# Kernel tuning notes

Hardware: AMD Instinct MI355X
Metric: run time of the kernel (lower is better)

## Reference

```python
import jax, jax.numpy as jnp
import numpy as np

NF, D, H, HD, NL, FF = 5, 64, 8, 8, 2, 128   # features, d_model, heads, head_dim, layers, ffn
NQ, QL, NC = 8, 3, 3                          # qubits, quantum layers, classes


def pos_encoding(S, d):
    pos = np.arange(S, dtype=np.float32)[:, None]
    div = np.exp(np.arange(0, d, 2, dtype=np.float32) * (-np.log(10000.0) / d))
    pe = np.zeros((S, d), np.float32)
    pe[:, 0::2] = np.sin(pos * div)
    pe[:, 1::2] = np.cos(pos * div)
    return jnp.asarray(pe)


def layernorm(x, g, b, eps=1e-5):
    m = x.mean(-1, keepdims=True)
    v = ((x - m) ** 2).mean(-1, keepdims=True)
    return (x - m) * jax.lax.rsqrt(v + eps) * g + b


def apply1q(psi, U, w):
    # psi: (2,)*NQ complex state; apply 2x2 gate U on wire w
    p = jnp.moveaxis(psi, w, 0)
    sh = p.shape
    p = (U @ p.reshape(2, -1)).reshape(sh)
    return jnp.moveaxis(p, 0, w)


def cnot(psi, c, t):
    p = jnp.moveaxis(psi, (c, t), (0, 1))
    sh = p.shape
    p = p.reshape(2, 2, -1)
    p = jnp.stack([p[0], p[1, ::-1]], 0).reshape(sh)  # flip target when control=1
    return jnp.moveaxis(p, (0, 1), (c, t))


def rx_mat(t):
    c, s = jnp.cos(t / 2), jnp.sin(t / 2)
    return jnp.stack([jnp.stack([c + 0j, -1j * s]), jnp.stack([-1j * s, c + 0j])]).astype(jnp.complex64)


def rot_mat(phi, th, om):
    # qml.Rot = RZ(om) RY(th) RZ(phi)
    c, s = jnp.cos(th / 2), jnp.sin(th / 2)
    return jnp.stack([
        jnp.stack([jnp.exp(-0.5j * (phi + om)) * c, -jnp.exp(0.5j * (phi - om)) * s]),
        jnp.stack([jnp.exp(-0.5j * (phi - om)) * s, jnp.exp(0.5j * (phi + om)) * c]),
    ]).astype(jnp.complex64)


def quantum_circuit(angles, weights):
    # angles: [NQ], weights: [QL, NQ, 3]. Circuit: QL x (AngleEmbedding(RX) + StronglyEntanglingLayer(range=1))
    psi = jnp.zeros((2,) * NQ, jnp.complex64).at[(0,) * NQ].set(1.0)
    for l in range(QL):
        for w in range(NQ):
            psi = apply1q(psi, rx_mat(angles[w]), w)
        for w in range(NQ):
            psi = apply1q(psi, rot_mat(weights[l, w, 0], weights[l, w, 1], weights[l, w, 2]), w)
        for w in range(NQ):
            psi = cnot(psi, w, (w + 1) % NQ)
    prob = jnp.abs(psi) ** 2
    zs = []
    for w in range(NC):  # <Z_w> = p(0_w) - p(1_w)
        marg = prob.sum(axis=tuple(i for i in range(NQ) if i != w))
        zs.append(marg[0] - marg[1])
    # von Neumann entropy of wires 0..3 (trace out wires 4..7), natural log
    mat = psi.reshape(16, 16)
    rho = mat @ mat.conj().T
    ev = jnp.clip(jnp.linalg.eigvalsh(rho), 1e-10, 1.0)
    ent = -jnp.sum(ev * jnp.log(ev))
    return jnp.stack(zs), ent


def setup_inputs() -> dict:
    key = jax.random.key(0)
    ks = jax.random.split(key, 30)
    sc = 0.02
    inp = {
        'x': jax.random.normal(ks[0], (16, 1024, NF), jnp.float32),
        'Wemb': sc * jax.random.normal(ks[1], (NF, D)), 'bemb': jnp.zeros((D,)),
        'Wq': sc * jax.random.normal(ks[2], (NL, D, D)), 'bq': jnp.zeros((NL, D)),
        'Wk': sc * jax.random.normal(ks[3], (NL, D, D)), 'bk': jnp.zeros((NL, D)),
        'Wv': sc * jax.random.normal(ks[4], (NL, D, D)), 'bv': jnp.zeros((NL, D)),
        'Wo': sc * jax.random.normal(ks[5], (NL, D, D)), 'bo': jnp.zeros((NL, D)),
        'ln1g': jnp.ones((NL, D)), 'ln1b': jnp.zeros((NL, D)),
        'ln2g': jnp.ones((NL, D)), 'ln2b': jnp.zeros((NL, D)),
        'Wf1': sc * jax.random.normal(ks[6], (NL, D, FF)), 'bf1': jnp.zeros((NL, FF)),
        'Wf2': sc * jax.random.normal(ks[7], (NL, FF, D)), 'bf2': jnp.zeros((NL, D)),
        'Wp1': sc * jax.random.normal(ks[8], (D, 32)), 'bp1': jnp.zeros((32,)),
        'Wp2': sc * jax.random.normal(ks[9], (32, NQ)), 'bp2': jnp.zeros((NQ,)),
        'qweights': jax.random.normal(ks[10], (QL, NQ, 3)),
    }
    return inp


def reference(x, Wemb, bemb, Wq, bq, Wk, bk, Wv, bv, Wo, bo, ln1g, ln1b, ln2g, ln2b,
              Wf1, bf1, Wf2, bf2, Wp1, bp1, Wp2, bp2, qweights):
    B, S, _ = x.shape
    h = x @ Wemb + bemb + pos_encoding(S, D)[None]  # aug + dropout are identity in eval
    scale = np.float32(1.0 / np.sqrt(HD))
    for l in range(NL):
        q = (h @ Wq[l] + bq[l]).reshape(B, S, H, HD).transpose(0, 2, 1, 3)
        k = (h @ Wk[l] + bk[l]).reshape(B, S, H, HD).transpose(0, 2, 1, 3)
        v = (h @ Wv[l] + bv[l]).reshape(B, S, H, HD).transpose(0, 2, 1, 3)
        att = jax.nn.softmax(jnp.einsum('bhsd,bhtd->bhst', q, k) * scale, axis=-1)
        o = jnp.einsum('bhst,bhtd->bhsd', att, v).transpose(0, 2, 1, 3).reshape(B, S, D)
        h = layernorm(h + o @ Wo[l] + bo[l], ln1g[l], ln1b[l])
        ff = jax.nn.relu(h @ Wf1[l] + bf1[l]) @ Wf2[l] + bf2[l]
        h = layernorm(h + ff, ln2g[l], ln2b[l])
    pooled = h.mean(1)
    feats = jax.nn.relu(pooled @ Wp1 + bp1) @ Wp2 + bp2
    angles = jnp.tanh(feats) * np.float32(np.pi)
    logits, ent = jax.vmap(quantum_circuit, in_axes=(0, None))(angles, qweights)
    return logits, ent
```

## Files before the change

### kernel.cpp

```cpp
#include <hip/hip_runtime.h>
#include <math.h>

#define BB 16
#define SS 1024
#define NF 5
#define DD 64
#define HH 8
#define HDIM 8
#define NLAYER 2
#define FFD 128
#define NQ 8
#define QLAY 3
#define NC 3
#define NSWEEP 5

typedef __fp16 hf2 __attribute__((ext_vector_type(2)));
typedef __fp16 h8  __attribute__((ext_vector_type(8)));
typedef float  f4x __attribute__((ext_vector_type(4)));

__device__ __forceinline__ int   f2i_(float x) { union { float f; int i; } u; u.f = x; return u.i; }
__device__ __forceinline__ float i2f_(int x)   { union { float f; int i; } u; u.i = x; return u.f; }

__device__ __forceinline__ float bperm_(int pa, float x) {
    return i2f_(__builtin_amdgcn_ds_bpermute(pa, f2i_(x)));
}

__device__ __forceinline__ float half32_(float x) {
#if defined(__has_builtin)
#if __has_builtin(__builtin_amdgcn_permlane32_swap)
    int xi = f2i_(x);
    auto r = __builtin_amdgcn_permlane32_swap(xi, xi, false, false);
    int r0 = (int)r[0], r1 = (int)r[1];
    return i2f_(r0 == xi ? r1 : r0);
#else
    return __shfl_xor(x, 32);
#endif
#else
    return __shfl_xor(x, 32);
#endif
}

template<int M> __device__ __forceinline__ float lx(float x) {
    if constexpr (M == 0) {
        return x;
    } else if constexpr (M == 1) {
        return i2f_(__builtin_amdgcn_update_dpp(0, f2i_(x), 0xB1, 0xF, 0xF, true));
    } else if constexpr (M == 2) {
        return i2f_(__builtin_amdgcn_update_dpp(0, f2i_(x), 0x4E, 0xF, 0xF, true));
    } else if constexpr (M == 3) {
        return i2f_(__builtin_amdgcn_update_dpp(0, f2i_(x), 0x1B, 0xF, 0xF, true));
    } else if constexpr (M < 32) {
        return i2f_(__builtin_amdgcn_ds_swizzle(f2i_(x), (M << 10) | 0x1F));
    } else {
        return lx<M & 31>(half32_(x));
    }
}

__device__ __forceinline__ float half16_(float x) {
#if defined(__has_builtin)
#if __has_builtin(__builtin_amdgcn_permlane16_swap)
    int xi = f2i_(x);
    auto r = __builtin_amdgcn_permlane16_swap(xi, xi, false, false);
    int r0 = (int)r[0], r1 = (int)r[1];
    return i2f_(r0 == xi ? r1 : r0);
#else
    return lx<16>(x);
#endif
#else
    return lx<16>(x);
#endif
}

__device__ __forceinline__ float wsum64_(float v) {
    v += half32_(v);
    v += half16_(v);
    v += lx<8>(v);
    v += lx<4>(v);
    v += lx<2>(v);
    v += lx<1>(v);
    return v;
}

#if defined(__has_builtin)
#if __has_builtin(__builtin_amdgcn_exp2f)
#define EXP2F(x) __builtin_amdgcn_exp2f(x)
#else
#define EXP2F(x) exp2f(x)
#endif
#else
#define EXP2F(x) exp2f(x)
#endif

#define QSCALE (0.3535533906f * 1.4426950408889634f)

__global__ __launch_bounds__(64) void k_qkv0(const float* __restrict__ x,
                                             const float* __restrict__ Wemb,
                                             const float* __restrict__ bemb,
                                             const float* __restrict__ Wq, const float* __restrict__ bq,
                                             const float* __restrict__ Wk, const float* __restrict__ bk,
                                             const float* __restrict__ Wv, const float* __restrict__ bv,
                                             hf2* __restrict__ qh, hf2* __restrict__ kh,
                                             hf2* __restrict__ vt, float* __restrict__ h) {
    __shared__ float hrow[4][DD];
    int d   = threadIdx.x;
    int bs0 = blockIdx.x * 4;
    {
        int i = d >> 1;
        float div = expf((float)(2 * i) * (-9.210340371976184f / 64.0f));
#pragma unroll
        for (int r = 0; r < 4; ++r) {
            int bs = bs0 + r;
            int s  = bs & (SS - 1);
            const float* xr = x + bs * NF;
            float acc = bemb[d];
#pragma unroll
            for (int f = 0; f < NF; ++f) acc += xr[f] * Wemb[f * DD + d];
            float ang = (float)s * div;
            float pe = (d & 1) ? cosf(ang) : sinf(ang);
            float hv = acc + pe;
            hrow[r][d] = hv;
            h[bs * DD + d] = hv;
        }
    }
    __syncthreads();
    const float* wq = Wq;
    const float* wk = Wk;
    const float* wv = Wv;
    float aq[4], ak[4], av[4];
    float bqv = bq[d], bkv = bk[d], bvv = bv[d];
#pragma unroll
    for (int r = 0; r < 4; ++r) { aq[r] = bqv; ak[r] = bkv; av[r] = bvv; }
#pragma unroll 4
    for (int i = 0; i < DD; ++i) {
        float wqv = wq[i * DD + d], wkv = wk[i * DD + d], wvv = wv[i * DD + d];
#pragma unroll
        for (int r = 0; r < 4; ++r) {
            float hv = hrow[r][i];
            aq[r] += hv * wqv; ak[r] += hv * wkv; av[r] += hv * wvv;
        }
    }
    int hh = d >> 3, hd = d & 7;
    const float qs = QSCALE;
    float aqp[4], akp[4];
#pragma unroll
    for (int r = 0; r < 4; ++r) { aqp[r] = lx<1>(aq[r]); akp[r] = lx<1>(ak[r]); }
    if ((hd & 1) == 0) {
#pragma unroll
        for (int r = 0; r < 4; ++r) {
            int bs = bs0 + r;
            int b = bs >> 10, s = bs & 1023;
            int bhs = ((b * HH + hh) << 10) | s;
            qh[bhs * 4 + (hd >> 1)] = __builtin_amdgcn_cvt_pkrtz(aq[r] * qs, aqp[r] * qs);
            kh[bhs * 4 + (hd >> 1)] = __builtin_amdgcn_cvt_pkrtz(ak[r], akp[r]);
        }
    }
    {
        int b = bs0 >> 10, s0 = bs0 & 1023;
        int vrow = (b * HH + hh) * 8 + hd;
        hf2* vp = vt + vrow * 512 + (s0 >> 1);
        vp[0] = __builtin_amdgcn_cvt_pkrtz(av[0], av[1]);
        vp[1] = __builtin_amdgcn_cvt_pkrtz(av[2], av[3]);
    }
}

__global__ __launch_bounds__(256) void k_attn(const float4* __restrict__ qh4,
                                              const float4* __restrict__ kh4,
                                              const float4* __restrict__ vt4,
                                              float* __restrict__ Ao) {
    int bh  = blockIdx.x;
    int sb  = blockIdx.y;
    int tid = threadIdx.x;
    int wv  = tid >> 6;
    int L   = tid & 63;
    int m = L & 15, quad = L >> 4;
    union U { float4 f; h8 h; };
    h8 hz = {0,0,0,0,0,0,0,0};
    h8 bQ = hz;
    if (quad == 0) { U u; u.f = qh4[(bh << 10) | (sb * 64 + wv * 16 + m)]; bQ = u.h; }
    int kmap = 8 * (m >> 2) + (m & 3);
    const float4* kbase = kh4 + (bh << 10);
    const float4* vbase = vt4 + ((bh * 8 + (m & 7)) << 7);
    f4x Oacc = {0.f, 0.f, 0.f, 0.f};
    float ls = 0.f;
    for (int kc = 0; kc < 32; ++kc) {
        h8 aK0 = hz, aK1 = hz;
        if (quad == 0) {
            U u0, u1;
            u0.f = kbase[kc * 32 + kmap];
            u1.f = kbase[kc * 32 + kmap + 4];
            aK0 = u0.h; aK1 = u1.h;
        }
        f4x S0 = {0.f,0.f,0.f,0.f}, S1 = {0.f,0.f,0.f,0.f};
        S0 = __builtin_amdgcn_mfma_f32_16x16x32_f16(aK0, bQ, S0, 0, 0, 0);
        S1 = __builtin_amdgcn_mfma_f32_16x16x32_f16(aK1, bQ, S1, 0, 0, 0);
        float p0 = EXP2F(S0[0]), p1 = EXP2F(S0[1]);
        float p2 = EXP2F(S0[2]), p3 = EXP2F(S0[3]);
        float p4 = EXP2F(S1[0]), p5 = EXP2F(S1[1]);
        float p6 = EXP2F(S1[2]), p7 = EXP2F(S1[3]);
        ls += (p0 + p1 + p2 + p3) + (p4 + p5 + p6 + p7);
        hf2 c0 = __builtin_amdgcn_cvt_pkrtz(p0, p1);
        hf2 c1 = __builtin_amdgcn_cvt_pkrtz(p2, p3);
        hf2 c2 = __builtin_amdgcn_cvt_pkrtz(p4, p5);
        hf2 c3 = __builtin_amdgcn_cvt_pkrtz(p6, p7);
        h8 aP;
        aP[0] = c0[0]; aP[1] = c0[1]; aP[2] = c1[0]; aP[3] = c1[1];
        aP[4] = c2[0]; aP[5] = c2[1]; aP[6] = c3[0]; aP[7] = c3[1];
        h8 bV = hz;
        if (m < 8) {
            U uv; uv.f = vbase[kc * 4 + quad];
            bV = uv.h;
        }
        Oacc = __builtin_amdgcn_mfma_f32_16x16x32_f16(aP, bV, Oacc, 0, 0, 0);
    }
    ls += half16_(ls);
    ls += half32_(ls);
    float d0 = bperm_((4 * quad + 0) << 2, ls);
    float d1 = bperm_((4 * quad + 1) << 2, ls);
    float d2 = bperm_((4 * quad + 2) << 2, ls);
    float d3 = bperm_((4 * quad + 3) << 2, ls);
    if (m < 8) {
        int srow = sb * 64 + wv * 16 + quad * 4;
        int base = (((bh << 10) | srow) << 3) + m;
        Ao[base]      = Oacc[0] / d0;
        Ao[base + 8]  = Oacc[1] / d1;
        Ao[base + 16] = Oacc[2] / d2;
        Ao[base + 24] = Oacc[3] / d3;
    }
}

__global__ __launch_bounds__(128) void k_mid(const float* __restrict__ Ao,
                                             const float* __restrict__ Wo, const float* __restrict__ bo,
                                             const float* __restrict__ g1, const float* __restrict__ b1,
                                             const float* __restrict__ Wf1, const float* __restrict__ bf1,
                                             const float* __restrict__ Wf2, const float* __restrict__ bf2,
                                             const float* __restrict__ g2, const float* __restrict__ b2,
                                             float* __restrict__ h, int l, int fuse,
                                             const float* __restrict__ Wq, const float* __restrict__ bq,
                                             const float* __restrict__ Wk, const float* __restrict__ bk,
                                             const float* __restrict__ Wv, const float* __restrict__ bv,
                                             hf2* __restrict__ qh, hf2* __restrict__ kh,
                                             hf2* __restrict__ vt, float* __restrict__ pp2) {
    __shared__ float orow[4][DD];
    __shared__ float h1s[4][DD];
    __shared__ float frow[4][FFD];
    __shared__ float hfin[4][DD];
    int t    = threadIdx.x;
    int d    = t & 63;
    int half = t >> 6;
    int bs0  = blockIdx.x * 4;
    int hh = d >> 3, hd = d & 7;
    int r0 = half * 2, r1 = r0 + 1;

#pragma unroll
    for (int rr = 0; rr < 2; ++rr) {
        int r  = r0 + rr;
        int bs = bs0 + r;
        int b = bs >> 10, s = bs & 1023;
        int bhs = ((b * HH + hh) << 10) | s;
        orow[r][d] = Ao[(bhs << 3) + hd];
    }
    __syncthreads();

    {
        const float* w = Wo + l * DD * DD;
        float bias = bo[l * DD + d];
        float acc0 = bias, acc1 = bias;
#pragma unroll 4
        for (int i = 0; i < DD; ++i) {
            float wv = w[i * DD + d];
            acc0 += orow[r0][i] * wv;
            acc1 += orow[r1][i] * wv;
        }
        float gg = g1[l * DD + d], bb = b1[l * DD + d];
        float accs[2] = {acc0, acc1};
#pragma unroll
        for (int rr = 0; rr < 2; ++rr) {
            int r = r0 + rr;
            float a = accs[rr] + h[(bs0 + r) * DD + d];
            float sum = wsum64_(a);
            float mean = sum * (1.f / 64.f);
            float dx = a - mean;
            float vs = wsum64_(dx * dx);
            float rstd = rsqrtf(vs * (1.f / 64.f) + 1e-5f);
            h1s[r][d] = dx * rstd * gg + bb;
        }
    }
    __syncthreads();

    {
        const float* w = Wf1 + l * DD * FFD;
        float bv_ = bf1[l * FFD + t];
        float a0 = bv_, a1 = bv_, a2 = bv_, a3 = bv_;
#pragma unroll 4
        for (int i = 0; i < DD; ++i) {
            float wv = w[i * FFD + t];
            a0 += h1s[0][i]*wv; a1 += h1s[1][i]*wv;
            a2 += h1s[2][i]*wv; a3 += h1s[3][i]*wv;
        }
        frow[0][t] = fmaxf(a0, 0.f); frow[1][t] = fmaxf(a1, 0.f);
        frow[2][t] = fmaxf(a2, 0.f); frow[3][t] = fmaxf(a3, 0.f);
    }
    __syncthreads();

    {
        const float* w = Wf2 + l * FFD * DD;
        float bias = bf2[l * DD + d];
        float acc0 = bias, acc1 = bias;
#pragma unroll 4
        for (int i = 0; i < FFD; ++i) {
            float wv = w[i * DD + d];
            acc0 += frow[r0][i] * wv;
            acc1 += frow[r1][i] * wv;
        }
        float gg = g2[l * DD + d], bb = b2[l * DD + d];
        float accs[2] = {acc0, acc1};
#pragma unroll
        for (int rr = 0; rr < 2; ++rr) {
            int r = r0 + rr;
            float a = accs[rr] + h1s[r][d];
            float sum = wsum64_(a);
            float mean = sum * (1.f / 64.f);
            float dx = a - mean;
            float vs = wsum64_(dx * dx);
            float rstd = rsqrtf(vs * (1.f / 64.f) + 1e-5f);
            float hv = dx * rstd * gg + bb;
            hfin[r][d] = hv;
            h[(bs0 + r) * DD + d] = hv;
        }
    }

    if (!fuse) {
        __syncthreads();
        if (t < 64) {
            pp2[blockIdx.x * DD + t] = (hfin[0][t] + hfin[1][t]) + (hfin[2][t] + hfin[3][t]);
        }
        return;
    }

    __syncthreads();
    const int l1 = l + 1;
    if (t < 64) {
        const float* wq = Wq + l1 * DD * DD;
        const float* wk = Wk + l1 * DD * DD;
        float aq[4], ak[4];
        float bqv = bq[l1 * DD + d], bkv = bk[l1 * DD + d];
#pragma unroll
        for (int r = 0; r < 4; ++r) { aq[r] = bqv; ak[r] = bkv; }
#pragma unroll 4
        for (int i = 0; i < DD; ++i) {
            float wqv = wq[i * DD + d], wkv = wk[i * DD + d];
#pragma unroll
            for (int r = 0; r < 4; ++r) {
                float hv = hfin[r][i];
                aq[r] += hv * wqv; ak[r] += hv * wkv;
            }
        }
        const float qs = QSCALE;
        float aqp[4], akp[4];
#pragma unroll
        for (int r = 0; r < 4; ++r) { aqp[r] = lx<1>(aq[r]); akp[r] = lx<1>(ak[r]); }
        if ((hd & 1) == 0) {
#pragma unroll
            for (int r = 0; r < 4; ++r) {
                int bs = bs0 + r;
                int b = bs >> 10, s = bs & 1023;
                int bhs = ((b * HH + hh) << 10) | s;
                qh[bhs * 4 + (hd >> 1)] = __builtin_amdgcn_cvt_pkrtz(aq[r] * qs, aqp[r] * qs);
                kh[bhs * 4 + (hd >> 1)] = __builtin_amdgcn_cvt_pkrtz(ak[r], akp[r]);
            }
        }
    } else {
        const float* wv = Wv + l1 * DD * DD;
        float av[4];
        float bvv = bv[l1 * DD + d];
#pragma unroll
        for (int r = 0; r < 4; ++r) av[r] = bvv;
#pragma unroll 4
        for (int i = 0; i < DD; ++i) {
            float wvv = wv[i * DD + d];
#pragma unroll
            for (int r = 0; r < 4; ++r) av[r] += hfin[r][i] * wvv;
        }
        int b = bs0 >> 10, s0 = bs0 & 1023;
        int vrow = (b * HH + hh) * 8 + hd;
        hf2* vp = vt + vrow * 512 + (s0 >> 1);
        vp[0] = __builtin_amdgcn_cvt_pkrtz(av[0], av[1]);
        vp[1] = __builtin_amdgcn_cvt_pkrtz(av[2], av[3]);
    }
}

__global__ __launch_bounds__(256) void k_tail(const float* __restrict__ pp2,
                                              const float* __restrict__ Wp1, const float* __restrict__ bp1,
                                              const float* __restrict__ Wp2, const float* __restrict__ bp2,
                                              const float* __restrict__ qw,
                                              float* __restrict__ out) {
    __shared__ float part[4][DD];
    __shared__ float pool_s[DD];
    __shared__ float hid[32];
    __shared__ float ang_s[NQ];
    __shared__ float ucoef[QLAY * 16][8];
    __shared__ float2 Ps2[256];
    int b = blockIdx.x; int t = threadIdx.x;
    int L = t;
    int lb4 = (t & 63) << 2;

    {
        int d = t & 63, ch = t >> 6;
        const float* pp = pp2 + (b * 256 + ch * 64) * DD + d;
        float acc = 0.f;
#pragma unroll 8
        for (int j = 0; j < 64; ++j) acc += pp[j * DD];
        part[ch][d] = acc;
    }
    __syncthreads();
    if (t < 64) pool_s[t] = (part[0][t] + part[1][t] + part[2][t] + part[3][t]) * (1.f / 1024.f);
    __syncthreads();
    if (t < 32) {
        float a = bp1[t];
#pragma unroll 8
        for (int i = 0; i < DD; ++i) a += pool_s[i] * Wp1[i * 32 + t];
        hid[t] = fmaxf(a, 0.f);
    }
    __syncthreads();
    if (t < NQ) {
        float a = bp2[t];
#pragma unroll 8
        for (int j = 0; j < 32; ++j) a += hid[j] * Wp2[j * NQ + t];
        ang_s[t] = tanhf(a) * 3.14159265358979f;
    }
    __syncthreads();

    if (t < QLAY * 16) {
        int l = t >> 4, g8 = t & 15, w = g8 & 7;
        float u00r, u00i, u01r, u01i, u10r, u10i, u11r, u11i;
        if (g8 < 8) {
            float ha = 0.5f * ang_s[w];
            float c = __cosf(ha), s = __sinf(ha);
            u00r = c;   u00i = 0.f; u01r = 0.f; u01i = -s;
            u10r = 0.f; u10i = -s;  u11r = c;   u11i = 0.f;
        } else {
            const float* p3 = qw + (l * NQ + w) * 3;
            float phi = p3[0], th = p3[1], om = p3[2];
            float ct = __cosf(0.5f * th), st = __sinf(0.5f * th);
            float al = 0.5f * (phi + om), be = 0.5f * (phi - om);
            float ca = __cosf(al), sa = __sinf(al), cb = __cosf(be), sb = __sinf(be);
            u00r =  ct * ca; u00i = -ct * sa;
            u01r = -st * cb; u01i = -st * sb;
            u10r =  st * cb; u10i = -st * sb;
            u11r =  ct * ca; u11i =  ct * sa;
        }
        float* up = ucoef[t];
        up[0] = u00r; up[1] = u00i; up[2] = u01r; up[3] = u01i;
        up[4] = u10r; up[5] = u10i; up[6] = u11r; up[7] = u11i;
    }
    __syncthreads();

    float ar[4], ai[4];
#pragma unroll
    for (int r = 0; r < 4; ++r) { ar[r] = 0.f; ai[r] = 0.f; }
    if (L == 0) ar[0] = 1.f;

    if (t < 64) {
#pragma unroll 1
        for (int l = 0; l < QLAY; ++l) {
#pragma unroll 1
            for (int g8 = 0; g8 < 16; ++g8) {
                const float* up = ucoef[(l << 4) | g8];
                float u00r = up[0], u00i = up[1], u01r = up[2], u01i = up[3];
                float u10r = up[4], u10i = up[5], u11r = up[6], u11i = up[7];
                int p = 7 - (g8 & 7);
                if (p >= 6) {
#pragma unroll
                    for (int pi_ = 0; pi_ < 2; ++pi_) {
                        int lo = (p == 7) ? pi_ : pi_ * 2;
                        int hi = (p == 7) ? pi_ + 2 : pi_ * 2 + 1;
                        float r0 = ar[lo], m0 = ai[lo], r1 = ar[hi], m1 = ai[hi];
                        ar[lo] = u00r*r0 - u00i*m0 + u01r*r1 - u01i*m1;
                        ai[lo] = u00r*m0 + u00i*r0 + u01r*m1 + u01i*r1;
                        ar[hi] = u10r*r0 - u10i*m0 + u11r*r1 - u11i*m1;
                        ai[hi] = u10r*m0 + u10i*r0 + u11r*m1 + u11i*r1;
                    }
                } else {
                    int bit = (L >> p) & 1;
                    float car = bit ? u11r : u00r, cai = bit ? u11i : u00i;
                    float cpr = bit ? u10r : u01r, cpi = bit ? u10i : u01i;
                    float pre[4], pim[4];
                    if (p == 5) {
#pragma unroll
                        for (int r = 0; r < 4; ++r) { pre[r] = half32_(ar[r]); pim[r] = half32_(ai[r]); }
                    } else if (p == 4) {
#pragma unroll
                        for (int r = 0; r < 4; ++r) { pre[r] = half16_(ar[r]); pim[r] = half16_(ai[r]); }
                    } else if (p == 3) {
#pragma unroll
                        for (int r = 0; r < 4; ++r) { pre[r] = lx<8>(ar[r]); pim[r] = lx<8>(ai[r]); }
                    } else if (p == 2) {
#pragma unroll
                        for (int r = 0; r < 4; ++r) { pre[r] = lx<4>(ar[r]); pim[r] = lx<4>(ai[r]); }
                    } else if (p == 1) {
#pragma unroll
                        for (int r = 0; r < 4; ++r) { pre[r] = lx<2>(ar[r]); pim[r] = lx<2>(ai[r]); }
                    } else {
#pragma unroll
                        for (int r = 0; r < 4; ++r) { pre[r] = lx<1>(ar[r]); pim[r] = lx<1>(ai[r]); }
                    }
#pragma unroll
                    for (int r = 0; r < 4; ++r) {
                        float nr = car*ar[r] - cai*ai[r] + cpr*pre[r] - cpi*pim[r];
                        float ni = car*ai[r] + cai*ar[r] + cpr*pim[r] + cpi*pre[r];
                        ar[r] = nr; ai[r] = ni;
                    }
                }
            }
            { float t0=ar[2]; ar[2]=ar[3]; ar[3]=t0; t0=ai[2]; ai[2]=ai[3]; ai[3]=t0; }
            ar[1] = half32_(ar[1]); ai[1] = half32_(ai[1]);
            ar[3] = half32_(ar[3]); ai[3] = half32_(ai[3]);
#pragma unroll 1
            for (int w = 2; w <= 6; ++w) {
                int pc = 7 - w, pt = 6 - w;
                bool ctrl = (L >> pc) & 1;
                float swr[4], swi[4];
                if (pt == 4) {
#pragma unroll
                    for (int r = 0; r < 4; ++r) { swr[r] = half16_(ar[r]); swi[r] = half16_(ai[r]); }
                } else if (pt == 3) {
#pragma unroll
                    for (int r = 0; r < 4; ++r) { swr[r] = lx<8>(ar[r]); swi[r] = lx<8>(ai[r]); }
                } else if (pt == 2) {
#pragma unroll
                    for (int r = 0; r < 4; ++r) { swr[r] = lx<4>(ar[r]); swi[r] = lx<4>(ai[r]); }
                } else if (pt == 1) {
#pragma unroll
                    for (int r = 0; r < 4; ++r) { swr[r] = lx<2>(ar[r]); swi[r] = lx<2>(ai[r]); }
                } else {
#pragma unroll
                    for (int r = 0; r < 4; ++r) { swr[r] = lx<1>(ar[r]); swi[r] = lx<1>(ai[r]); }
                }
#pragma unroll
                for (int r = 0; r < 4; ++r) {
                    ar[r] = ctrl ? swr[r] : ar[r];
                    ai[r] = ctrl ? swi[r] : ai[r];
                }
            }
            {
                bool ctrl = L & 1;
                float n0r = ctrl ? ar[2] : ar[0], n2r = ctrl ? ar[0] : ar[2];
                float n0i = ctrl ? ai[2] : ai[0], n2i = ctrl ? ai[0] : ai[2];
                float n1r = ctrl ? ar[3] : ar[1], n3r = ctrl ? ar[1] : ar[3];
                float n1i = ctrl ? ai[3] : ai[1], n3i = ctrl ? ai[1] : ai[3];
                ar[0]=n0r; ar[1]=n1r; ar[2]=n2r; ar[3]=n3r;
                ai[0]=n0i; ai[1]=n1i; ai[2]=n2i; ai[3]=n3i;
            }
        }

        {
            float p0 = ar[0]*ar[0]+ai[0]*ai[0];
            float p1 = ar[1]*ar[1]+ai[1]*ai[1];
            float p2 = ar[2]*ar[2]+ai[2]*ai[2];
            float p3 = ar[3]*ar[3]+ai[3]*ai[3];
            float z0 = p0 + p1 - p2 - p3;
            float z1 = p0 - p1 + p2 - p3;
            float zs = p0 + p1 + p2 + p3;
            float z2 = (L & 32) ? -zs : zs;
            z0 += lx<1>(z0);   z1 += lx<1>(z1);   z2 += lx<1>(z2);
            z0 += lx<2>(z0);   z1 += lx<2>(z1);   z2 += lx<2>(z2);
            z0 += lx<4>(z0);   z1 += lx<4>(z1);   z2 += lx<4>(z2);
            z0 += lx<8>(z0);   z1 += lx<8>(z1);   z2 += lx<8>(z2);
            z0 += half16_(z0); z1 += half16_(z1); z2 += half16_(z2);
            z0 += half32_(z0); z1 += half32_(z1); z2 += half32_(z2);
            if (L == 0) {
                out[b * NC + 0] = z0;
                out[b * NC + 1] = z1;
                out[b * NC + 2] = z2;
            }
        }

#pragma unroll
        for (int r = 0; r < 4; ++r) Ps2[(r << 6) | L] = make_float2(ar[r], ai[r]);
    }
    __syncthreads();

    if (t < 64) {
        int c   = L >> 2;
        int seg = L & 3;
        float gr[4], gi[4];
#pragma unroll
        for (int j = 0; j < 4; ++j) {
            float2 tv = Ps2[(seg * 4 + j) * 16 + c];
            gr[j] = tv.x; gi[j] = tv.y;
        }
        float alm = 0.f;
#pragma unroll
        for (int j = 0; j < 4; ++j) alm += gr[j]*gr[j] + gi[j]*gi[j];
        alm += lx<1>(alm);
        alm += lx<2>(alm);

#pragma unroll 1
        for (int sweep = 0; sweep < NSWEEP; ++sweep) {
#pragma unroll 1
            for (int m = 1; m <= 15; ++m) {
                int xm = m << 2;
                float pgr[4], pgi[4], bep;
                if ((xm & 12) == 0) {
                    if (xm == 16) {
#pragma unroll
                        for (int j = 0; j < 4; ++j) { pgr[j] = half16_(gr[j]); pgi[j] = half16_(gi[j]); }
                        bep = half16_(alm);
                    } else if (xm == 32) {
#pragma unroll
                        for (int j = 0; j < 4; ++j) { pgr[j] = half32_(gr[j]); pgi[j] = half32_(gi[j]); }
                        bep = half32_(alm);
                    } else {
#pragma unroll
                        for (int j = 0; j < 4; ++j) {
                            pgr[j] = half16_(half32_(gr[j]));
                            pgi[j] = half16_(half32_(gi[j]));
                        }
                        bep = half16_(half32_(alm));
                    }
                } else {
                    int pa = lb4 ^ (xm << 2);
#pragma unroll
                    for (int j = 0; j < 4; ++j) {
                        pgr[j] = bperm_(pa, gr[j]);
                        pgi[j] = bperm_(pa, gi[j]);
                    }
                    bep = bperm_(pa, alm);
                }
                float d = 0.f, e = 0.f;
#pragma unroll
                for (int j = 0; j < 4; ++j) {
                    d += gr[j]*pgr[j] + gi[j]*pgi[j];
                    e += gr[j]*pgi[j] - gi[j]*pgr[j];
                }
                d += lx<1>(d); e += lx<1>(e);
                d += lx<2>(d); e += lx<2>(e);
                float g2 = d*d + e*e;
                float cth = 1.f, sth = 0.f, cph = 1.f, sph = 0.f, gn = 0.f;
                if (g2 > 1e-26f) {
                    gn = __builtin_amdgcn_sqrtf(g2);
                    float ginv = __builtin_amdgcn_rcpf(gn);
                    cph = d * ginv; sph = -e * ginv;
                    float tau = (alm - bep) * (0.5f * ginv);
                    float rr = __builtin_amdgcn_rsqf(1.f + tau*tau);
                    float co = fminf(fabsf(tau) * rr, 1.0f);
                    cth = __builtin_amdgcn_sqrtf(0.5f + 0.5f*co);
                    sth = copysignf(__builtin_amdgcn_sqrtf(0.5f - 0.5f*co), tau);
                }
#pragma unroll
                for (int j = 0; j < 4; ++j) {
                    float er = cph*pgr[j] - sph*pgi[j];
                    float ei = cph*pgi[j] + sph*pgr[j];
                    gr[j] = cth * gr[j] + sth * er;
                    gi[j] = cth * gi[j] + sth * ei;
                }
                alm = cth*cth*alm + sth*sth*bep + 2.f*cth*sth*gn;
            }
        }

        float alm2 = 0.f;
#pragma unroll
        for (int j = 0; j < 4; ++j) alm2 += gr[j]*gr[j] + gi[j]*gi[j];
        alm2 += lx<1>(alm2);
        alm2 += lx<2>(alm2);

        float ev = fminf(fmaxf(alm2, 1e-10f), 1.0f);
        float term = -ev * __logf(ev);
        term += lx<4>(term);
        term += lx<8>(term);
        term += half16_(term);
        term += half32_(term);
        if (L == 0) out[BB * NC + b] = term;
    }
}

extern "C" void kernel_launch(void* const* d_in, const int* in_sizes, int n_in,
                              void* d_out, int out_size, void* d_ws, size_t ws_size,
                              hipStream_t stream) {
    const float* x    = (const float*)d_in[0];
    const float* Wemb = (const float*)d_in[1];
    const float* bemb = (const float*)d_in[2];
    const float* Wq   = (const float*)d_in[3];
    const float* bq   = (const float*)d_in[4];
    const float* Wk   = (const float*)d_in[5];
    const float* bk   = (const float*)d_in[6];
    const float* Wv   = (const float*)d_in[7];
    const float* bv   = (const float*)d_in[8];
    const float* Wo   = (const float*)d_in[9];
    const float* bo   = (const float*)d_in[10];
    const float* ln1g = (const float*)d_in[11];
    const float* ln1b = (const float*)d_in[12];
    const float* ln2g = (const float*)d_in[13];
    const float* ln2b = (const float*)d_in[14];
    const float* Wf1  = (const float*)d_in[15];
    const float* bf1  = (const float*)d_in[16];
    const float* Wf2  = (const float*)d_in[17];
    const float* bf2  = (const float*)d_in[18];
    const float* Wp1  = (const float*)d_in[19];
    const float* bp1  = (const float*)d_in[20];
    const float* Wp2  = (const float*)d_in[21];
    const float* bp2  = (const float*)d_in[22];
    const float* qwts = (const float*)d_in[23];
    float* out = (float*)d_out;

    const size_t M = 1u << 20;
    float* ws   = (float*)d_ws;
    float* h    = ws;
    hf2*   qh   = (hf2*)(ws + M);
    hf2*   kh   = (hf2*)(ws + M + M / 2);
    hf2*   vt   = (hf2*)(ws + 2 * M);
    float* Ao   = ws + 2 * M + M / 2;
    float* pp2  = ws + 3 * M + M / 2;

    k_qkv0<<<BB * SS / 4, 64, 0, stream>>>(x, Wemb, bemb, Wq, bq, Wk, bk, Wv, bv,
                                           qh, kh, vt, h);
    k_attn<<<dim3(BB * HH, 16), 256, 0, stream>>>((const float4*)qh, (const float4*)kh,
                                                  (const float4*)vt, Ao);
    k_mid<<<BB * SS / 4, 128, 0, stream>>>(Ao, Wo, bo, ln1g, ln1b,
                                           Wf1, bf1, Wf2, bf2, ln2g, ln2b, h, 0, 1,
                                           Wq, bq, Wk, bk, Wv, bv, qh, kh, vt, pp2);
    k_attn<<<dim3(BB * HH, 16), 256, 0, stream>>>((const float4*)qh, (const float4*)kh,
                                                  (const float4*)vt, Ao);
    k_mid<<<BB * SS / 4, 128, 0, stream>>>(Ao, Wo, bo, ln1g, ln1b,
                                           Wf1, bf1, Wf2, bf2, ln2g, ln2b, h, 1, 0,
                                           Wq, bq, Wk, bk, Wv, bv, qh, kh, vt, pp2);
    k_tail<<<BB, 256, 0, stream>>>(pp2, Wp1, bp1, Wp2, bp2, qwts, out);
}
```

Baseline: 292.4 us.

## Run tail kernel as single 1024-thread block with one wavefront per batch

The tail kernel changes from 16 blocks of 256 threads to one block of 1024 threads, with each 64-lane wavefront handling one batch element. The pooling reduction now uses float4 loads and cross-lane reductions instead of a shared-memory partial-sum stage, and no lanes sit idle during the quantum simulation. This reduces per-block overhead and idle threads, but puts all the tail work on a single compute unit, which may add latency where 16 blocks previously ran in parallel across CUs.

```diff
diff --git a/kernel.cpp b/kernel.cpp
--- a/kernel.cpp
+++ b/kernel.cpp
@@ -389,52 +389,61 @@
     }
 }
 
-__global__ __launch_bounds__(256) void k_tail(const float* __restrict__ pp2,
-                                              const float* __restrict__ Wp1, const float* __restrict__ bp1,
-                                              const float* __restrict__ Wp2, const float* __restrict__ bp2,
-                                              const float* __restrict__ qw,
-                                              float* __restrict__ out) {
-    __shared__ float part[4][DD];
-    __shared__ float pool_s[DD];
-    __shared__ float hid[32];
-    __shared__ float ang_s[NQ];
-    __shared__ float ucoef[QLAY * 16][8];
-    __shared__ float2 Ps2[256];
-    int b = blockIdx.x; int t = threadIdx.x;
-    int L = t;
-    int lb4 = (t & 63) << 2;
+__global__ __launch_bounds__(1024) void k_tail(const float* __restrict__ pp2,
+                                               const float* __restrict__ Wp1, const float* __restrict__ bp1,
+                                               const float* __restrict__ Wp2, const float* __restrict__ bp2,
+                                               const float* __restrict__ qw,
+                                               float* __restrict__ out) {
+    __shared__ float pool_s[BB][DD];
+    __shared__ float hid_s[BB][32];
+    __shared__ float ang_s[BB][NQ];
+    __shared__ float ucoef[BB][QLAY * 16][8];
+    __shared__ float2 Ps2[BB][256];
+    int t = threadIdx.x;
+    int b = t >> 6;
+    int L = t & 63;
+    int lb4 = L << 2;
 
     {
-        int d = t & 63, ch = t >> 6;
-        const float* pp = pp2 + (b * 256 + ch * 64) * DD + d;
-        float acc = 0.f;
+        int dq4 = L & 15;
+        int j0  = (L >> 4) << 6;
+        const float4* pp4 = (const float4*)pp2 + (((b << 8) + j0) << 4) + dq4;
+        float ax = 0.f, ay = 0.f, az = 0.f, aw = 0.f;
 #pragma unroll 8
-        for (int j = 0; j < 64; ++j) acc += pp[j * DD];
-        part[ch][d] = acc;
-    }
-    __syncthreads();
-    if (t < 64) pool_s[t] = (part[0][t] + part[1][t] + part[2][t] + part[3][t]) * (1.f / 1024.f);
-    __syncthreads();
-    if (t < 32) {
-        float a = bp1[t];
+        for (int j = 0; j < 64; ++j) {
+            float4 v = pp4[j << 4];
+            ax += v.x; ay += v.y; az += v.z; aw += v.w;
+        }
+        ax += half16_(ax); ay += half16_(ay); az += half16_(az); aw += half16_(aw);
+        ax += half32_(ax); ay += half32_(ay); az += half32_(az); aw += half32_(aw);
+        if (L < 16) {
+            pool_s[b][L * 4 + 0] = ax * (1.f / 1024.f);
+            pool_s[b][L * 4 + 1] = ay * (1.f / 1024.f);
+            pool_s[b][L * 4 + 2] = az * (1.f / 1024.f);
+            pool_s[b][L * 4 + 3] = aw * (1.f / 1024.f);
+        }
+    }
+    __syncthreads();
+    if (L < 32) {
+        float a = bp1[L];
 #pragma unroll 8
-        for (int i = 0; i < DD; ++i) a += pool_s[i] * Wp1[i * 32 + t];
-        hid[t] = fmaxf(a, 0.f);
-    }
-    __syncthreads();
-    if (t < NQ) {
-        float a = bp2[t];
+        for (int i = 0; i < DD; ++i) a += pool_s[b][i] * Wp1[i * 32 + L];
+        hid_s[b][L] = fmaxf(a, 0.f);
+    }
+    __syncthreads();
+    if (L < NQ) {
+        float a = bp2[L];
 #pragma unroll 8
-        for (int j = 0; j < 32; ++j) a += hid[j] * Wp2[j * NQ + t];
-        ang_s[t] = tanhf(a) * 3.14159265358979f;
-    }
-    __syncthreads();
-
-    if (t < QLAY * 16) {
-        int l = t >> 4, g8 = t & 15, w = g8 & 7;
+        for (int j = 0; j < 32; ++j) a += hid_s[b][j] * Wp2[j * NQ + L];
+        ang_s[b][L] = tanhf(a) * 3.14159265358979f;
+    }
+    __syncthreads();
+
+    if (L < QLAY * 16) {
+        int l = L >> 4, g8 = L & 15, w = g8 & 7;
         float u00r, u00i, u01r, u01i, u10r, u10i, u11r, u11i;
         if (g8 < 8) {
-            float ha = 0.5f * ang_s[w];
+            float ha = 0.5f * ang_s[b][w];
             float c = __cosf(ha), s = __sinf(ha);
             u00r = c;   u00i = 0.f; u01r = 0.f; u01i = -s;
             u10r = 0.f; u10i = -s;  u11r = c;   u11i = 0.f;
@@ -449,7 +458,7 @@
             u10r =  st * cb; u10i = -st * sb;
             u11r =  ct * ca; u11i =  ct * sa;
         }
-        float* up = ucoef[t];
+        float* up = ucoef[b][L];
         up[0] = u00r; up[1] = u00i; up[2] = u01r; up[3] = u01i;
         up[4] = u10r; up[5] = u10i; up[6] = u11r; up[7] = u11i;
     }
@@ -460,133 +469,131 @@
     for (int r = 0; r < 4; ++r) { ar[r] = 0.f; ai[r] = 0.f; }
     if (L == 0) ar[0] = 1.f;
 
-    if (t < 64) {
 #pragma unroll 1
-        for (int l = 0; l < QLAY; ++l) {
+    for (int l = 0; l < QLAY; ++l) {
 #pragma unroll 1
-            for (int g8 = 0; g8 < 16; ++g8) {
-                const float* up = ucoef[(l << 4) | g8];
-                float u00r = up[0], u00i = up[1], u01r = up[2], u01i = up[3];
-                float u10r = up[4], u10i = up[5], u11r = up[6], u11i = up[7];
-                int p = 7 - (g8 & 7);
-                if (p >= 6) {
-#pragma unroll
-                    for (int pi_ = 0; pi_ < 2; ++pi_) {
-                        int lo = (p == 7) ? pi_ : pi_ * 2;
-                        int hi = (p == 7) ? pi_ + 2 : pi_ * 2 + 1;
-                        float r0 = ar[lo], m0 = ai[lo], r1 = ar[hi], m1 = ai[hi];
-                        ar[lo] = u00r*r0 - u00i*m0 + u01r*r1 - u01i*m1;
-                        ai[lo] = u00r*m0 + u00i*r0 + u01r*m1 + u01i*r1;
-                        ar[hi] = u10r*r0 - u10i*m0 + u11r*r1 - u11i*m1;
-                        ai[hi] = u10r*m0 + u10i*r0 + u11r*m1 + u11i*r1;
-                    }
+        for (int g8 = 0; g8 < 16; ++g8) {
+            const float* up = ucoef[b][(l << 4) | g8];
+            float u00r = up[0], u00i = up[1], u01r = up[2], u01i = up[3];
+            float u10r = up[4], u10i = up[5], u11r = up[6], u11i = up[7];
+            int p = 7 - (g8 & 7);
+            if (p >= 6) {
+#pragma unroll
+                for (int pi_ = 0; pi_ < 2; ++pi_) {
+                    int lo = (p == 7) ? pi_ : pi_ * 2;
+                    int hi = (p == 7) ? pi_ + 2 : pi_ * 2 + 1;
+                    float r0 = ar[lo], m0 = ai[lo], r1 = ar[hi], m1 = ai[hi];
+                    ar[lo] = u00r*r0 - u00i*m0 + u01r*r1 - u01i*m1;
+                    ai[lo] = u00r*m0 + u00i*r0 + u01r*m1 + u01i*r1;
+                    ar[hi] = u10r*r0 - u10i*m0 + u11r*r1 - u11i*m1;
+                    ai[hi] = u10r*m0 + u10i*r0 + u11r*m1 + u11i*r1;
+                }
+            } else {
+                int bit = (L >> p) & 1;
+                float car = bit ? u11r : u00r, cai = bit ? u11i : u00i;
+                float cpr = bit ? u10r : u01r, cpi = bit ? u10i : u01i;
+                float pre[4], pim[4];
+                if (p == 5) {
+#pragma unroll
+                    for (int r = 0; r < 4; ++r) { pre[r] = half32_(ar[r]); pim[r] = half32_(ai[r]); }
+                } else if (p == 4) {
+#pragma unroll
+                    for (int r = 0; r < 4; ++r) { pre[r] = half16_(ar[r]); pim[r] = half16_(ai[r]); }
+                } else if (p == 3) {
+#pragma unroll
+                    for (int r = 0; r < 4; ++r) { pre[r] = lx<8>(ar[r]); pim[r] = lx<8>(ai[r]); }
+                } else if (p == 2) {
+#pragma unroll
+                    for (int r = 0; r < 4; ++r) { pre[r] = lx<4>(ar[r]); pim[r] = lx<4>(ai[r]); }
+                } else if (p == 1) {
+#pragma unroll
+                    for (int r = 0; r < 4; ++r) { pre[r] = lx<2>(ar[r]); pim[r] = lx<2>(ai[r]); }
                 } else {
-                    int bit = (L >> p) & 1;
-                    float car = bit ? u11r : u00r, cai = bit ? u11i : u00i;
-                    float cpr = bit ? u10r : u01r, cpi = bit ? u10i : u01i;
-                    float pre[4], pim[4];
-                    if (p == 5) {
-#pragma unroll
-                        for (int r = 0; r < 4; ++r) { pre[r] = half32_(ar[r]); pim[r] = half32_(ai[r]); }
-                    } else if (p == 4) {
-#pragma unroll
-                        for (int r = 0; r < 4; ++r) { pre[r] = half16_(ar[r]); pim[r] = half16_(ai[r]); }
-                    } else if (p == 3) {
-#pragma unroll
-                        for (int r = 0; r < 4; ++r) { pre[r] = lx<8>(ar[r]); pim[r] = lx<8>(ai[r]); }
-                    } else if (p == 2) {
-#pragma unroll
-                        for (int r = 0; r < 4; ++r) { pre[r] = lx<4>(ar[r]); pim[r] = lx<4>(ai[r]); }
-                    } else if (p == 1) {
-#pragma unroll
-                        for (int r = 0; r < 4; ++r) { pre[r] = lx<2>(ar[r]); pim[r] = lx<2>(ai[r]); }
-                    } else {
-#pragma unroll
-                        for (int r = 0; r < 4; ++r) { pre[r] = lx<1>(ar[r]); pim[r] = lx<1>(ai[r]); }
-                    }
-#pragma unroll
-                    for (int r = 0; r < 4; ++r) {
-                        float nr = car*ar[r] - cai*ai[r] + cpr*pre[r] - cpi*pim[r];
-                        float ni = car*ai[r] + cai*ar[r] + cpr*pim[r] + cpi*pre[r];
-                        ar[r] = nr; ai[r] = ni;
-                    }
+#pragma unroll
+                    for (int r = 0; r < 4; ++r) { pre[r] = lx<1>(ar[r]); pim[r] = lx<1>(ai[r]); }
+                }
+#pragma unroll
+                for (int r = 0; r < 4; ++r) {
+                    float nr = car*ar[r] - cai*ai[r] + cpr*pre[r] - cpi*pim[r];
+                    float ni = car*ai[r] + cai*ar[r] + cpr*pim[r] + cpi*pre[r];
+                    ar[r] = nr; ai[r] = ni;
                 }
             }
-            { float t0=ar[2]; ar[2]=ar[3]; ar[3]=t0; t0=ai[2]; ai[2]=ai[3]; ai[3]=t0; }
-            ar[1] = half32_(ar[1]); ai[1] = half32_(ai[1]);
-            ar[3] = half32_(ar[3]); ai[3] = half32_(ai[3]);
+        }
+        { float t0=ar[2]; ar[2]=ar[3]; ar[3]=t0; t0=ai[2]; ai[2]=ai[3]; ai[3]=t0; }
+        ar[1] = half32_(ar[1]); ai[1] = half32_(ai[1]);
+        ar[3] = half32_(ar[3]); ai[3] = half32_(ai[3]);
 #pragma unroll 1
-            for (int w = 2; w <= 6; ++w) {
-                int pc = 7 - w, pt = 6 - w;
-                bool ctrl = (L >> pc) & 1;
-                float swr[4], swi[4];
-                if (pt == 4) {
-#pragma unroll
-                    for (int r = 0; r < 4; ++r) { swr[r] = half16_(ar[r]); swi[r] = half16_(ai[r]); }
-                } else if (pt == 3) {
-#pragma unroll
-                    for (int r = 0; r < 4; ++r) { swr[r] = lx<8>(ar[r]); swi[r] = lx<8>(ai[r]); }
-                } else if (pt == 2) {
-#pragma unroll
-                    for (int r = 0; r < 4; ++r) { swr[r] = lx<4>(ar[r]); swi[r] = lx<4>(ai[r]); }
-                } else if (pt == 1) {
-#pragma unroll
-                    for (int r = 0; r < 4; ++r) { swr[r] = lx<2>(ar[r]); swi[r] = lx<2>(ai[r]); }
-                } else {
-#pragma unroll
-                    for (int r = 0; r < 4; ++r) { swr[r] = lx<1>(ar[r]); swi[r] = lx<1>(ai[r]); }
-                }
-#pragma unroll
-                for (int r = 0; r < 4; ++r) {
-                    ar[r] = ctrl ? swr[r] : ar[r];
-                    ai[r] = ctrl ? swi[r] : ai[r];
-                }
+        for (int w = 2; w <= 6; ++w) {
+            int pc = 7 - w, pt = 6 - w;
+            bool ctrl = (L >> pc) & 1;
+            float swr[4], swi[4];
+            if (pt == 4) {
+#pragma unroll
+                for (int r = 0; r < 4; ++r) { swr[r] = half16_(ar[r]); swi[r] = half16_(ai[r]); }
+            } else if (pt == 3) {
+#pragma unroll
+                for (int r = 0; r < 4; ++r) { swr[r] = lx<8>(ar[r]); swi[r] = lx<8>(ai[r]); }
+            } else if (pt == 2) {
+#pragma unroll
+                for (int r = 0; r < 4; ++r) { swr[r] = lx<4>(ar[r]); swi[r] = lx<4>(ai[r]); }
+            } else if (pt == 1) {
+#pragma unroll
+                for (int r = 0; r < 4; ++r) { swr[r] = lx<2>(ar[r]); swi[r] = lx<2>(ai[r]); }
+            } else {
+#pragma unroll
+                for (int r = 0; r < 4; ++r) { swr[r] = lx<1>(ar[r]); swi[r] = lx<1>(ai[r]); }
             }
-            {
-                bool ctrl = L & 1;
-                float n0r = ctrl ? ar[2] : ar[0], n2r = ctrl ? ar[0] : ar[2];
-                float n0i = ctrl ? ai[2] : ai[0], n2i = ctrl ? ai[0] : ai[2];
-                float n1r = ctrl ? ar[3] : ar[1], n3r = ctrl ? ar[1] : ar[3];
-                float n1i = ctrl ? ai[3] : ai[1], n3i = ctrl ? ai[1] : ai[3];
-                ar[0]=n0r; ar[1]=n1r; ar[2]=n2r; ar[3]=n3r;
-                ai[0]=n0i; ai[1]=n1i; ai[2]=n2i; ai[3]=n3i;
+#pragma unroll
+            for (int r = 0; r < 4; ++r) {
+                ar[r] = ctrl ? swr[r] : ar[r];
+                ai[r] = ctrl ? swi[r] : ai[r];
             }
         }
-
         {
-            float p0 = ar[0]*ar[0]+ai[0]*ai[0];
-            float p1 = ar[1]*ar[1]+ai[1]*ai[1];
-            float p2 = ar[2]*ar[2]+ai[2]*ai[2];
-            float p3 = ar[3]*ar[3]+ai[3]*ai[3];
-            float z0 = p0 + p1 - p2 - p3;
-            float z1 = p0 - p1 + p2 - p3;
-            float zs = p0 + p1 + p2 + p3;
-            float z2 = (L & 32) ? -zs : zs;
-            z0 += lx<1>(z0);   z1 += lx<1>(z1);   z2 += lx<1>(z2);
-            z0 += lx<2>(z0);   z1 += lx<2>(z1);   z2 += lx<2>(z2);
-            z0 += lx<4>(z0);   z1 += lx<4>(z1);   z2 += lx<4>(z2);
-            z0 += lx<8>(z0);   z1 += lx<8>(z1);   z2 += lx<8>(z2);
-            z0 += half16_(z0); z1 += half16_(z1); z2 += half16_(z2);
-            z0 += half32_(z0); z1 += half32_(z1); z2 += half32_(z2);
-            if (L == 0) {
-                out[b * NC + 0] = z0;
-                out[b * NC + 1] = z1;
-                out[b * NC + 2] = z2;
-            }
-        }
-
-#pragma unroll
-        for (int r = 0; r < 4; ++r) Ps2[(r << 6) | L] = make_float2(ar[r], ai[r]);
-    }
-    __syncthreads();
-
-    if (t < 64) {
+            bool ctrl = L & 1;
+            float n0r = ctrl ? ar[2] : ar[0], n2r = ctrl ? ar[0] : ar[2];
+            float n0i = ctrl ? ai[2] : ai[0], n2i = ctrl ? ai[0] : ai[2];
+            float n1r = ctrl ? ar[3] : ar[1], n3r = ctrl ? ar[1] : ar[3];
+            float n1i = ctrl ? ai[3] : ai[1], n3i = ctrl ? ai[1] : ai[3];
+            ar[0]=n0r; ar[1]=n1r; ar[2]=n2r; ar[3]=n3r;
+            ai[0]=n0i; ai[1]=n1i; ai[2]=n2i; ai[3]=n3i;
+        }
+    }
+
+    {
+        float p0 = ar[0]*ar[0]+ai[0]*ai[0];
+        float p1 = ar[1]*ar[1]+ai[1]*ai[1];
+        float p2 = ar[2]*ar[2]+ai[2]*ai[2];
+        float p3 = ar[3]*ar[3]+ai[3]*ai[3];
+        float z0 = p0 + p1 - p2 - p3;
+        float z1 = p0 - p1 + p2 - p3;
+        float zs = p0 + p1 + p2 + p3;
+        float z2 = (L & 32) ? -zs : zs;
+        z0 += lx<1>(z0);   z1 += lx<1>(z1);   z2 += lx<1>(z2);
+        z0 += lx<2>(z0);   z1 += lx<2>(z1);   z2 += lx<2>(z2);
+        z0 += lx<4>(z0);   z1 += lx<4>(z1);   z2 += lx<4>(z2);
+        z0 += lx<8>(z0);   z1 += lx<8>(z1);   z2 += lx<8>(z2);
+        z0 += half16_(z0); z1 += half16_(z1); z2 += half16_(z2);
+        z0 += half32_(z0); z1 += half32_(z1); z2 += half32_(z2);
+        if (L == 0) {
+            out[b * NC + 0] = z0;
+            out[b * NC + 1] = z1;
+            out[b * NC + 2] = z2;
+        }
+    }
+
+#pragma unroll
+    for (int r = 0; r < 4; ++r) Ps2[b][(r << 6) | L] = make_float2(ar[r], ai[r]);
+    __syncthreads();
+
+    {
         int c   = L >> 2;
         int seg = L & 3;
         float gr[4], gi[4];
 #pragma unroll
         for (int j = 0; j < 4; ++j) {
-            float2 tv = Ps2[(seg * 4 + j) * 16 + c];
+            float2 tv = Ps2[b][(seg * 4 + j) * 16 + c];
             gr[j] = tv.x; gi[j] = tv.y;
         }
         float alm = 0.f;
@@ -724,5 +731,5 @@
     k_mid<<<BB * SS / 4, 128, 0, stream>>>(Ao, Wo, bo, ln1g, ln1b,
                                            Wf1, bf1, Wf2, bf2, ln2g, ln2b, h, 1, 0,
                                            Wq, bq, Wk, bk, Wv, bv, qh, kh, vt, pp2);
-    k_tail<<<BB, 256, 0, stream>>>(pp2, Wp1, bp1, Wp2, bp2, qwts, out);
-}
+    k_tail<<<1, 1024, 0, stream>>>(pp2, Wp1, bp1, Wp2, bp2, qwts, out);
+}
```

Measured after the change: 350.6 us. 19.9% more time.

## Use DPP row-mirror shuffles in Jacobi sweep and vectorize tail pooling

Applied to the files above, without the earlier changes.

The Jacobi eigen-sweep in the tail kernel now uses composed DPP row_mirror/half_mirror and permlane swaps for the lane exchange instead of ds_bpermute and ds_swizzle, which avoids LDS-path latency. The mean-pool reduction switches to float4 loads across 16 groups, and the fixed Rot-gate coefficients are computed by otherwise idle threads alongside pooling rather than after it. These changes are aimed at cutting latency in the serial single-block-per-batch tail. The cost is more ALU ops per exchange where DPP steps are chained, plus some added code complexity.

```diff
diff --git a/kernel.cpp b/kernel.cpp
--- a/kernel.cpp
+++ b/kernel.cpp
@@ -40,6 +40,21 @@
 #endif
 }
 
+__device__ __forceinline__ float half16_(float x) {
+#if defined(__has_builtin)
+#if __has_builtin(__builtin_amdgcn_permlane16_swap)
+    int xi = f2i_(x);
+    auto r = __builtin_amdgcn_permlane16_swap(xi, xi, false, false);
+    int r0 = (int)r[0], r1 = (int)r[1];
+    return i2f_(r0 == xi ? r1 : r0);
+#else
+    return i2f_(__builtin_amdgcn_ds_swizzle(f2i_(x), (16 << 10) | 0x1F));
+#endif
+#else
+    return i2f_(__builtin_amdgcn_ds_swizzle(f2i_(x), (16 << 10) | 0x1F));
+#endif
+}
+
 template<int M> __device__ __forceinline__ float lx(float x) {
     if constexpr (M == 0) {
         return x;
@@ -49,26 +64,19 @@
         return i2f_(__builtin_amdgcn_update_dpp(0, f2i_(x), 0x4E, 0xF, 0xF, true));
     } else if constexpr (M == 3) {
         return i2f_(__builtin_amdgcn_update_dpp(0, f2i_(x), 0x1B, 0xF, 0xF, true));
+    } else if constexpr (M == 7) {
+        return i2f_(__builtin_amdgcn_update_dpp(0, f2i_(x), 0x141, 0xF, 0xF, true));
+    } else if constexpr (M == 15) {
+        return i2f_(__builtin_amdgcn_update_dpp(0, f2i_(x), 0x140, 0xF, 0xF, true));
+    } else if constexpr (M < 8) {
+        return lx<M ^ 7>(lx<7>(x));
+    } else if constexpr (M < 16) {
+        return lx<M ^ 15>(lx<15>(x));
     } else if constexpr (M < 32) {
-        return i2f_(__builtin_amdgcn_ds_swizzle(f2i_(x), (M << 10) | 0x1F));
+        return lx<M & 15>(half16_(x));
     } else {
         return lx<M & 31>(half32_(x));
     }
-}
-
-__device__ __forceinline__ float half16_(float x) {
-#if defined(__has_builtin)
-#if __has_builtin(__builtin_amdgcn_permlane16_swap)
-    int xi = f2i_(x);
-    auto r = __builtin_amdgcn_permlane16_swap(xi, xi, false, false);
-    int r0 = (int)r[0], r1 = (int)r[1];
-    return i2f_(r0 == xi ? r1 : r0);
-#else
-    return lx<16>(x);
-#endif
-#else
-    return lx<16>(x);
-#endif
 }
 
 __device__ __forceinline__ float wsum64_(float v) {
@@ -394,30 +402,57 @@
                                               const float* __restrict__ Wp2, const float* __restrict__ bp2,
                                               const float* __restrict__ qw,
                                               float* __restrict__ out) {
-    __shared__ float part[4][DD];
+    __shared__ float4 part4[16][16];
     __shared__ float pool_s[DD];
     __shared__ float hid[32];
     __shared__ float ang_s[NQ];
     __shared__ float ucoef[QLAY * 16][8];
     __shared__ float2 Ps2[256];
     int b = blockIdx.x; int t = threadIdx.x;
-    int L = t;
-    int lb4 = (t & 63) << 2;
+    int L = t & 63;
+
+    if (t >= 64 && t < 64 + QLAY * NQ) {
+        int e = t - 64; int l = e >> 3, w = e & 7;
+        const float* p3 = qw + (l * NQ + w) * 3;
+        float phi = p3[0], th = p3[1], om = p3[2];
+        float ct = __cosf(0.5f * th), st = __sinf(0.5f * th);
+        float al = 0.5f * (phi + om), be = 0.5f * (phi - om);
+        float ca = __cosf(al), sa = __sinf(al), cb = __cosf(be), sb = __sinf(be);
+        float* up = ucoef[l * 16 + 8 + w];
+        up[0] =  ct * ca; up[1] = -ct * sa;
+        up[2] = -st * cb; up[3] = -st * sb;
+        up[4] =  st * cb; up[5] = -st * sb;
+        up[6] =  ct * ca; up[7] =  ct * sa;
+    }
 
     {
-        int d = t & 63, ch = t >> 6;
-        const float* pp = pp2 + (b * 256 + ch * 64) * DD + d;
-        float acc = 0.f;
-#pragma unroll 8
-        for (int j = 0; j < 64; ++j) acc += pp[j * DD];
-        part[ch][d] = acc;
-    }
-    __syncthreads();
-    if (t < 64) pool_s[t] = (part[0][t] + part[1][t] + part[2][t] + part[3][t]) * (1.f / 1024.f);
+        int dq = t & 15, g = t >> 4;
+        const float4* pp4 = (const float4*)pp2 + ((b * 256 + g * 16) << 4) + dq;
+        float ax = 0.f, ay = 0.f, az = 0.f, aw = 0.f;
+#pragma unroll
+        for (int j = 0; j < 16; ++j) {
+            float4 v = pp4[j << 4];
+            ax += v.x; ay += v.y; az += v.z; aw += v.w;
+        }
+        part4[g][dq] = make_float4(ax, ay, az, aw);
+    }
+    __syncthreads();
+    if (t < 16) {
+        float ax = 0.f, ay = 0.f, az = 0.f, aw = 0.f;
+#pragma unroll
+        for (int g = 0; g < 16; ++g) {
+            float4 v = part4[g][t];
+            ax += v.x; ay += v.y; az += v.z; aw += v.w;
+        }
+        pool_s[t * 4 + 0] = ax * (1.f / 1024.f);
+        pool_s[t * 4 + 1] = ay * (1.f / 1024.f);
+        pool_s[t * 4 + 2] = az * (1.f / 1024.f);
+        pool_s[t * 4 + 3] = aw * (1.f / 1024.f);
+    }
     __syncthreads();
     if (t < 32) {
         float a = bp1[t];
-#pragma unroll 8
+#pragma unroll 16
         for (int i = 0; i < DD; ++i) a += pool_s[i] * Wp1[i * 32 + t];
         hid[t] = fmaxf(a, 0.f);
     }
@@ -429,38 +464,22 @@
         ang_s[t] = tanhf(a) * 3.14159265358979f;
     }
     __syncthreads();
-
-    if (t < QLAY * 16) {
-        int l = t >> 4, g8 = t & 15, w = g8 & 7;
-        float u00r, u00i, u01r, u01i, u10r, u10i, u11r, u11i;
-        if (g8 < 8) {
-            float ha = 0.5f * ang_s[w];
-            float c = __cosf(ha), s = __sinf(ha);
-            u00r = c;   u00i = 0.f; u01r = 0.f; u01i = -s;
-            u10r = 0.f; u10i = -s;  u11r = c;   u11i = 0.f;
-        } else {
-            const float* p3 = qw + (l * NQ + w) * 3;
-            float phi = p3[0], th = p3[1], om = p3[2];
-            float ct = __cosf(0.5f * th), st = __sinf(0.5f * th);
-            float al = 0.5f * (phi + om), be = 0.5f * (phi - om);
-            float ca = __cosf(al), sa = __sinf(al), cb = __cosf(be), sb = __sinf(be);
-            u00r =  ct * ca; u00i = -ct * sa;
-            u01r = -st * cb; u01i = -st * sb;
-            u10r =  st * cb; u10i = -st * sb;
-            u11r =  ct * ca; u11i =  ct * sa;
-        }
-        float* up = ucoef[t];
-        up[0] = u00r; up[1] = u00i; up[2] = u01r; up[3] = u01i;
-        up[4] = u10r; up[5] = u10i; up[6] = u11r; up[7] = u11i;
-    }
-    __syncthreads();
-
-    float ar[4], ai[4];
-#pragma unroll
-    for (int r = 0; r < 4; ++r) { ar[r] = 0.f; ai[r] = 0.f; }
-    if (L == 0) ar[0] = 1.f;
+    if (t < QLAY * NQ) {
+        int l = t >> 3, w = t & 7;
+        float ha = 0.5f * ang_s[w];
+        float c = __cosf(ha), s = __sinf(ha);
+        float* up = ucoef[l * 16 + w];
+        up[0] = c;   up[1] = 0.f; up[2] = 0.f; up[3] = -s;
+        up[4] = 0.f; up[5] = -s;  up[6] = c;   up[7] = 0.f;
+    }
+    __syncthreads();
 
     if (t < 64) {
+        float ar[4], ai[4];
+#pragma unroll
+        for (int r = 0; r < 4; ++r) { ar[r] = 0.f; ai[r] = 0.f; }
+        if (L == 0) ar[0] = 1.f;
+
 #pragma unroll 1
         for (int l = 0; l < QLAY; ++l) {
 #pragma unroll 1
@@ -600,41 +619,38 @@
 #pragma unroll 1
             for (int m = 1; m <= 15; ++m) {
                 int xm = m << 2;
-                float pgr[4], pgi[4], bep;
-                if ((xm & 12) == 0) {
-                    if (xm == 16) {
-#pragma unroll
-                        for (int j = 0; j < 4; ++j) { pgr[j] = half16_(gr[j]); pgi[j] = half16_(gi[j]); }
-                        bep = half16_(alm);
-                    } else if (xm == 32) {
-#pragma unroll
-                        for (int j = 0; j < 4; ++j) { pgr[j] = half32_(gr[j]); pgi[j] = half32_(gi[j]); }
-                        bep = half32_(alm);
-                    } else {
-#pragma unroll
-                        for (int j = 0; j < 4; ++j) {
-                            pgr[j] = half16_(half32_(gr[j]));
-                            pgi[j] = half16_(half32_(gi[j]));
-                        }
-                        bep = half16_(half32_(alm));
-                    }
-                } else {
-                    int pa = lb4 ^ (xm << 2);
-#pragma unroll
-                    for (int j = 0; j < 4; ++j) {
-                        pgr[j] = bperm_(pa, gr[j]);
-                        pgi[j] = bperm_(pa, gi[j]);
-                    }
-                    bep = bperm_(pa, alm);
+                float pv[9];
+#pragma unroll
+                for (int j = 0; j < 4; ++j) { pv[j] = gr[j]; pv[4 + j] = gi[j]; }
+                pv[8] = alm;
+                int lowm = xm & 12;
+                if (lowm == 4) {
+#pragma unroll
+                    for (int j = 0; j < 9; ++j) pv[j] = lx<4>(pv[j]);
+                } else if (lowm == 8) {
+#pragma unroll
+                    for (int j = 0; j < 9; ++j) pv[j] = lx<8>(pv[j]);
+                } else if (lowm == 12) {
+#pragma unroll
+                    for (int j = 0; j < 9; ++j) pv[j] = lx<12>(pv[j]);
+                }
+                if (xm & 16) {
+#pragma unroll
+                    for (int j = 0; j < 9; ++j) pv[j] = half16_(pv[j]);
+                }
+                if (xm & 32) {
+#pragma unroll
+                    for (int j = 0; j < 9; ++j) pv[j] = half32_(pv[j]);
                 }
                 float d = 0.f, e = 0.f;
 #pragma unroll
                 for (int j = 0; j < 4; ++j) {
-                    d += gr[j]*pgr[j] + gi[j]*pgi[j];
-                    e += gr[j]*pgi[j] - gi[j]*pgr[j];
+                    d += gr[j]*pv[j] + gi[j]*pv[4 + j];
+                    e += gr[j]*pv[4 + j] - gi[j]*pv[j];
                 }
                 d += lx<1>(d); e += lx<1>(e);
                 d += lx<2>(d); e += lx<2>(e);
+                float bep = pv[8];
                 float g2 = d*d + e*e;
                 float cth = 1.f, sth = 0.f, cph = 1.f, sph = 0.f, gn = 0.f;
                 if (g2 > 1e-26f) {
@@ -649,8 +665,8 @@
                 }
 #pragma unroll
                 for (int j = 0; j < 4; ++j) {
-                    float er = cph*pgr[j] - sph*pgi[j];
-                    float ei = cph*pgi[j] + sph*pgr[j];
+                    float er = cph*pv[j] - sph*pv[4 + j];
+                    float ei = cph*pv[4 + j] + sph*pv[j];
                     gr[j] = cth * gr[j] + sth * er;
                     gi[j] = cth * gi[j] + sth * ei;
                 }
```

New measurement: 298.3 us. +2.0%, slower.
